# Kernel tuning notes

Measured on AMD Instinct MI355X. Metric: run time of the kernel, lower is better.

## Reference

```python
import jax, jax.numpy as jnp
import numpy as np

B, S, H, HD = 8, 1024, 16, 64
D = H * HD
NINF = -10000.0
EPS = 1e-6


def setup_inputs() -> dict:
    key = jax.random.key(0)
    ks = jax.random.split(key, 6)
    std = 0.02
    return {
        "x": jax.random.normal(ks[0], (B, S, D), jnp.float32),
        "mask": jax.random.randint(ks[1], (B, S), 0, 2, jnp.int32),
        "wq": jax.random.normal(ks[2], (D, D), jnp.float32) * std,
        "bq": jnp.zeros((D,), jnp.float32),
        "wk": jax.random.normal(ks[3], (D, D), jnp.float32) * std,
        "bk": jnp.zeros((D,), jnp.float32),
        "wv": jax.random.normal(ks[4], (D, D), jnp.float32) * std,
        "bv": jnp.zeros((D,), jnp.float32),
        "wo": jax.random.normal(ks[5], (D, D), jnp.float32) * std,
        "bo": jnp.zeros((D,), jnp.float32),
        "gamma": jnp.ones((D,), jnp.float32),
        "beta": jnp.zeros((D,), jnp.float32),
    }


def _heads(t):
    # [B,S,D] -> [B,H,S,HD]
    return t.reshape(t.shape[0], t.shape[1], H, HD).transpose(0, 2, 1, 3)


def _layernorm(x, gamma, beta):
    mu = jnp.mean(x, -1, keepdims=True)
    var = jnp.mean(jnp.square(x - mu), -1, keepdims=True)
    return (x - mu) * jax.lax.rsqrt(var + EPS) * gamma + beta


def reference(x, mask, wq, bq, wk, bk, wv, bv, wo, bo, gamma, beta):
    q = _heads(x @ wq + bq)
    k = _heads(x @ wk + bk)
    v = _heads(x @ wv + bv)
    scores = jnp.einsum("bhqd,bhkd->bhqk", q, k) / np.sqrt(HD).astype(np.float32)
    # padding mask broadcast over key axis: 1 = masked
    scores = scores + mask.astype(jnp.float32)[:, None, None, :] * NINF
    attn = jax.nn.softmax(scores, axis=-1)
    ctx = jnp.einsum("bhqk,bhkd->bhqd", attn, v)  # [B,H,S,HD]
    ctx = ctx.transpose(0, 2, 1, 3).reshape(B, S, D)
    out = _layernorm(x + ctx @ wo + bo, gamma, beta)
    return out
```

## Files before the change

### kernel.cpp

```cpp
#include <hip/hip_runtime.h>
#include <stdint.h>

typedef unsigned short u16;
typedef unsigned int u32;
typedef __bf16 b16x8 __attribute__((ext_vector_type(8)));
typedef float f32x4 __attribute__((ext_vector_type(4)));

#define B_ 8
#define S_ 1024
#define H_ 16
#define HD_ 64
#define D_ 1024
#define M_ 8192

__device__ __forceinline__ u16 f2bf(float f) {
  u32 u = __float_as_uint(f);
  return (u16)((u + 0x7fffu + ((u >> 16) & 1u)) >> 16);
}
__device__ __forceinline__ u16 bfbits(float f) {
  union {
    __bf16 b;
    u16 u;
  } c;
  c.b = (__bf16)f;
  return c.u;
}

__device__ __forceinline__ f32x4 mfma16(b16x8 a, b16x8 b, f32x4 c) {
  return __builtin_amdgcn_mfma_f32_16x16x32_bf16(a, b, c, 0, 0, 0);
}

__device__ __forceinline__ void cp16(const u16* g, u16* l) {
  __builtin_amdgcn_global_load_lds(
      (const __attribute__((address_space(1))) u32*)(g),
      (__attribute__((address_space(3))) u32*)(l), 16, 0, 0);
}

__global__ __launch_bounds__(1024) void wconv_kernel(
    const float* __restrict__ w0, const float* __restrict__ w1,
    const float* __restrict__ w2, const float* __restrict__ w3,
    u16* __restrict__ t0, u16* __restrict__ t1, u16* __restrict__ t2,
    u16* __restrict__ t3) {
  __shared__ float tile[32][33];
  const int z = blockIdx.z;
  const float* src = (z == 0) ? w0 : (z == 1) ? w1 : (z == 2) ? w2 : w3;
  u16* dst = (z == 0) ? t0 : (z == 1) ? t1 : (z == 2) ? t2 : t3;
  const int tx = threadIdx.x, ty = threadIdx.y;
  const int x0 = blockIdx.x * 32, y0 = blockIdx.y * 32;
  tile[ty][tx] = src[(size_t)(y0 + ty) * D_ + x0 + tx];
  __syncthreads();
  dst[(size_t)(x0 + ty) * D_ + y0 + tx] = f2bf(tile[tx][ty]);
}

__global__ __launch_bounds__(256) void xconv_kernel(const float* __restrict__ x,
                                                    u16* __restrict__ xb) {
  const size_t i = ((size_t)blockIdx.x * 256 + threadIdx.x) * 4;
  const float4 v = *(const float4*)(x + i);
  u16 o[4] = {f2bf(v.x), f2bf(v.y), f2bf(v.z), f2bf(v.w)};
  uint2 pack;
  pack.x = ((u32)o[1] << 16) | o[0];
  pack.y = ((u32)o[3] << 16) | o[2];
  *(uint2*)(xb + i) = pack;
}

__device__ __forceinline__ void gemm128_mainloop(
    const u16* __restrict__ A, const u16* __restrict__ BT, int K, int m0,
    int n0, u16* lds, f32x4 (&acc)[4][4]) {
  const int t = threadIdx.x;
  const int lane = t & 63;
  const int w = t >> 6;
  const int l15 = lane & 15;
  const int q4 = lane >> 4;
  const int mwave = (w >> 1) * 64;
  const int nwave = (w & 1) * 64;

  u16* Alds = lds;
  u16* Blds = lds + 8192;

  const f32x4 zero = {0.f, 0.f, 0.f, 0.f};
  for (int mt = 0; mt < 4; ++mt)
    for (int nt = 0; nt < 4; ++nt) acc[mt][nt] = zero;

  const int rbase = t >> 3;
  const int scol = ((t & 7) ^ (rbase & 7)) * 8;
  const u16* Ag = A + (size_t)(m0 + rbase) * K + scol;
  const u16* Bg = BT + (size_t)(n0 + rbase) * K + scol;

  const int sx = l15 & 7;
  const int cA0 = ((0 * 4 + q4) ^ sx) * 8;
  const int cA1 = ((1 * 4 + q4) ^ sx) * 8;

  for (int k0 = 0; k0 < K; k0 += 64) {
    __syncthreads();
    for (int c = 0; c < 4; ++c) {
      cp16(Ag + (size_t)(c * 32) * K + k0, Alds + c * 2048 + t * 8);
      cp16(Bg + (size_t)(c * 32) * K + k0, Blds + c * 2048 + t * 8);
    }
    __syncthreads();

    b16x8 af[4][2], bfr[4][2];
    for (int mt = 0; mt < 4; ++mt) {
      const int row = (mwave + mt * 16 + l15) * 64;
      af[mt][0] = *(const b16x8*)(Alds + row + cA0);
      af[mt][1] = *(const b16x8*)(Alds + row + cA1);
    }
    for (int nt = 0; nt < 4; ++nt) {
      const int row = (nwave + nt * 16 + l15) * 64;
      bfr[nt][0] = *(const b16x8*)(Blds + row + cA0);
      bfr[nt][1] = *(const b16x8*)(Blds + row + cA1);
    }
    for (int mt = 0; mt < 4; ++mt)
      for (int nt = 0; nt < 4; ++nt) {
        acc[mt][nt] = mfma16(af[mt][0], bfr[nt][0], acc[mt][nt]);
        acc[mt][nt] = mfma16(af[mt][1], bfr[nt][1], acc[mt][nt]);
      }
  }
}

__global__ __launch_bounds__(256) void qkv_gemm_kernel(
    const u16* __restrict__ xb, const u16* __restrict__ wtq,
    const u16* __restrict__ wtk, const u16* __restrict__ wtv,
    const float* __restrict__ bq, const float* __restrict__ bk,
    const float* __restrict__ bv, u16* __restrict__ Q, u16* __restrict__ Kb,
    u16* __restrict__ VT) {
  __shared__ __align__(16) u16 lds[16384];
  const int z = blockIdx.z;
  const u16* BTp = (z == 0) ? wtq : (z == 1) ? wtk : wtv;
  const float* bias = (z == 0) ? bq : (z == 1) ? bk : bv;
  u16* out = (z == 0) ? Q : (z == 1) ? Kb : VT;
  const int m0 = blockIdx.y * 128, n0 = blockIdx.x * 128;

  f32x4 acc[4][4];
  gemm128_mainloop(xb, BTp, D_, m0, n0, lds, acc);

  const int lane = threadIdx.x & 63, w = threadIdx.x >> 6;
  const int l15 = lane & 15, q4 = lane >> 4;
  const int mwave = (w >> 1) * 64, nwave = (w & 1) * 64;

  for (int nt = 0; nt < 4; ++nt) {
    const int n = n0 + nwave + nt * 16 + l15;
    const float bias_v = bias[n];
    const int h = n >> 6, hd = n & 63;
    for (int mt = 0; mt < 4; ++mt) {
      for (int r = 0; r < 4; ++r) {
        const int m = m0 + mwave + mt * 16 + q4 * 4 + r;
        const int b = m >> 10, s = m & 1023;
        const float v = acc[mt][nt][r] + bias_v;
        size_t idx;
        if (z < 2)
          idx = (((size_t)(b * H_ + h)) * S_ + s) * HD_ + hd;
        else
          idx = (((size_t)(b * H_ + h)) * HD_ + hd) * S_ + s;
        out[idx] = f2bf(v);
      }
    }
  }
}

#define PAD_ 68
#define QPAD_ 72
__global__ __launch_bounds__(256) void attn_kernel(
    const u16* __restrict__ Q, const u16* __restrict__ Kb,
    const u16* __restrict__ VT, const int* __restrict__ mask,
    u16* __restrict__ ctx) {
  __shared__ __align__(16) u16 QPlds[64 * QPAD_];
  __shared__ __align__(16) u16 Klds[64 * PAD_];
  __shared__ __align__(16) u16 Vlds[64 * PAD_];
  __shared__ __align__(16) float Mlds[1024];

  const int t = threadIdx.x;
  const int lane = t & 63, w = t >> 6;
  const int l15 = lane & 15, q4 = lane >> 4;
  const int id = blockIdx.x;
  const int bh = id & 127;
  const int b = bh >> 4, h = bh & 15;
  const int q0 = (id >> 7) * 64;

  const u16* Qbh = Q + (size_t)bh * S_ * HD_;
  const u16* Kbh = Kb + (size_t)bh * S_ * HD_;
  const u16* Vbh = VT + (size_t)bh * S_ * HD_;
  const int* maskb = mask + b * S_;

  const int srow = t >> 3, scol = (t & 7) * 8;
  {
    b16x8 q0v = *(const b16x8*)(Qbh + (size_t)(q0 + srow) * HD_ + scol);
    b16x8 q1v = *(const b16x8*)(Qbh + (size_t)(q0 + srow + 32) * HD_ + scol);
    const int4 mv = *(const int4*)(maskb + t * 4);
    *(b16x8*)(QPlds + srow * QPAD_ + scol) = q0v;
    *(b16x8*)(QPlds + (srow + 32) * QPAD_ + scol) = q1v;
    float4 mf;
    mf.x = -14427.0f * (float)mv.x;
    mf.y = -14427.0f * (float)mv.y;
    mf.z = -14427.0f * (float)mv.z;
    mf.w = -14427.0f * (float)mv.w;
    *(float4*)(Mlds + t * 4) = mf;
  }
  __syncthreads();
  b16x8 aq[2];
  aq[0] = *(const b16x8*)(QPlds + (w * 16 + l15) * QPAD_ + q4 * 8);
  aq[1] = *(const b16x8*)(QPlds + (w * 16 + l15) * QPAD_ + 32 + q4 * 8);

  const f32x4 zero = {0.f, 0.f, 0.f, 0.f};
  f32x4 acc[4];
  for (int nt = 0; nt < 4; ++nt) acc[nt] = zero;
  float lsum = 0.f;
  u16* Pw = QPlds + w * 16 * QPAD_;
  const float c1 = 0.18033688f;

  b16x8 kv0 = *(const b16x8*)(Kbh + (size_t)srow * HD_ + scol);
  b16x8 kv1 = *(const b16x8*)(Kbh + (size_t)(srow + 32) * HD_ + scol);
  b16x8 vv0 = *(const b16x8*)(Vbh + (size_t)srow * S_ + scol);
  b16x8 vv1 = *(const b16x8*)(Vbh + (size_t)(srow + 32) * S_ + scol);

  for (int j = 0; j < 16; ++j) {
    const int key0 = j * 64;
    __syncthreads();
    *(b16x8*)(Klds + srow * PAD_ + scol) = kv0;
    *(b16x8*)(Klds + (srow + 32) * PAD_ + scol) = kv1;
    *(b16x8*)(Vlds + srow * PAD_ + scol) = vv0;
    *(b16x8*)(Vlds + (srow + 32) * PAD_ + scol) = vv1;
    __syncthreads();

    if (j < 15) {
      const int kn = key0 + 64;
      kv0 = *(const b16x8*)(Kbh + (size_t)(kn + srow) * HD_ + scol);
      kv1 = *(const b16x8*)(Kbh + (size_t)(kn + srow + 32) * HD_ + scol);
      vv0 = *(const b16x8*)(Vbh + (size_t)srow * S_ + kn + scol);
      vv1 = *(const b16x8*)(Vbh + (size_t)(srow + 32) * S_ + kn + scol);
    }

    f32x4 sf[4];
    for (int nt = 0; nt < 4; ++nt) sf[nt] = zero;
    for (int kk = 0; kk < 2; ++kk)
      for (int nt = 0; nt < 4; ++nt) {
        b16x8 bk =
            *(const b16x8*)(Klds + (nt * 16 + l15) * PAD_ + kk * 32 + q4 * 8);
        sf[nt] = mfma16(bk, aq[kk], sf[nt]);
      }

    for (int nt = 0; nt < 4; ++nt) {
      const float4 mk = *(const float4*)(Mlds + key0 + nt * 16 + q4 * 4);
      float p0 = __builtin_amdgcn_exp2f(sf[nt][0] * c1 + mk.x);
      float p1 = __builtin_amdgcn_exp2f(sf[nt][1] * c1 + mk.y);
      float p2 = __builtin_amdgcn_exp2f(sf[nt][2] * c1 + mk.z);
      float p3 = __builtin_amdgcn_exp2f(sf[nt][3] * c1 + mk.w);
      lsum += (p0 + p1) + (p2 + p3);
      uint2 pk;
      pk.x = ((u32)bfbits(p1) << 16) | bfbits(p0);
      pk.y = ((u32)bfbits(p3) << 16) | bfbits(p2);
      *(uint2*)(Pw + l15 * QPAD_ + nt * 16 + q4 * 4) = pk;
    }
    asm volatile("s_waitcnt lgkmcnt(0)" ::: "memory");

    for (int kk = 0; kk < 2; ++kk) {
      b16x8 bp = *(const b16x8*)(Pw + l15 * QPAD_ + kk * 32 + q4 * 8);
      for (int nt = 0; nt < 4; ++nt) {
        b16x8 vb =
            *(const b16x8*)(Vlds + (nt * 16 + l15) * PAD_ + kk * 32 + q4 * 8);
        acc[nt] = mfma16(vb, bp, acc[nt]);
      }
    }
  }

  lsum += __shfl_xor(lsum, 16);
  lsum += __shfl_xor(lsum, 32);
  const float inv = 1.0f / lsum;

  const int srw = q0 + w * 16 + l15;
  u16* crow = ctx + ((size_t)(b * S_ + srw)) * D_ + h * 64;
  for (int nt = 0; nt < 4; ++nt) {
    uint2 pk;
    pk.x = ((u32)bfbits(acc[nt][1] * inv) << 16) | bfbits(acc[nt][0] * inv);
    pk.y = ((u32)bfbits(acc[nt][3] * inv) << 16) | bfbits(acc[nt][2] * inv);
    *(uint2*)(crow + nt * 16 + q4 * 4) = pk;
  }
}

__global__ __launch_bounds__(256) void out_gemm_kernel(
    const u16* __restrict__ ctx, const u16* __restrict__ wto,
    const float* __restrict__ bo, const float* __restrict__ x,
    float* __restrict__ y) {
  __shared__ __align__(16) u16 lds[16384];
  const int m0 = blockIdx.y * 128, n0 = blockIdx.x * 128;
  f32x4 acc[4][4];
  gemm128_mainloop(ctx, wto, D_, m0, n0, lds, acc);

  const int lane = threadIdx.x & 63, w = threadIdx.x >> 6;
  const int l15 = lane & 15, q4 = lane >> 4;
  const int mwave = (w >> 1) * 64, nwave = (w & 1) * 64;

  for (int nt = 0; nt < 4; ++nt) {
    const int n = n0 + nwave + nt * 16 + l15;
    const float bias = bo[n];
    for (int mt = 0; mt < 4; ++mt) {
      for (int r = 0; r < 4; ++r) {
        const int m = m0 + mwave + mt * 16 + q4 * 4 + r;
        y[(size_t)m * D_ + n] = acc[mt][nt][r] + bias + x[(size_t)m * D_ + n];
      }
    }
  }
}

__global__ __launch_bounds__(256) void ln_kernel(const float* __restrict__ y,
                                                 const float* __restrict__ g,
                                                 const float* __restrict__ be,
                                                 float* __restrict__ out) {
  const int row = blockIdx.x, t = threadIdx.x;
  const float* yr = y + (size_t)row * D_;
  const float4 v = *(const float4*)(yr + t * 4);
  float s = v.x + v.y + v.z + v.w;
  float ss = v.x * v.x + v.y * v.y + v.z * v.z + v.w * v.w;
  for (int off = 1; off < 64; off <<= 1) {
    s += __shfl_xor(s, off);
    ss += __shfl_xor(ss, off);
  }
  __shared__ float red[8];
  const int w = t >> 6, lane = t & 63;
  if (lane == 0) {
    red[w] = s;
    red[4 + w] = ss;
  }
  __syncthreads();
  s = red[0] + red[1] + red[2] + red[3];
  ss = red[4] + red[5] + red[6] + red[7];
  const float mu = s * (1.f / 1024.f);
  const float var = ss * (1.f / 1024.f) - mu * mu;
  const float rs = rsqrtf(var + 1e-6f);
  const int c = t * 4;
  const float4 gv = *(const float4*)(g + c);
  const float4 bv = *(const float4*)(be + c);
  float4 o;
  o.x = (v.x - mu) * rs * gv.x + bv.x;
  o.y = (v.y - mu) * rs * gv.y + bv.y;
  o.z = (v.z - mu) * rs * gv.z + bv.z;
  o.w = (v.w - mu) * rs * gv.w + bv.w;
  *(float4*)(out + (size_t)row * D_ + c) = o;
}

extern "C" void kernel_launch(void* const* d_in, const int* in_sizes, int n_in,
                              void* d_out, int out_size, void* d_ws,
                              size_t ws_size, hipStream_t stream) {
  const float* x = (const float*)d_in[0];
  const int* mask = (const int*)d_in[1];
  const float* wq = (const float*)d_in[2];
  const float* bq = (const float*)d_in[3];
  const float* wk = (const float*)d_in[4];
  const float* bk = (const float*)d_in[5];
  const float* wv = (const float*)d_in[6];
  const float* bv = (const float*)d_in[7];
  const float* wo = (const float*)d_in[8];
  const float* bo = (const float*)d_in[9];
  const float* gamma = (const float*)d_in[10];
  const float* beta = (const float*)d_in[11];
  float* out = (float*)d_out;

  char* ws = (char*)d_ws;
  const size_t MB = 1024ull * 1024ull;
  u16* wtq = (u16*)(ws + 0 * MB);
  u16* wtk = (u16*)(ws + 2 * MB);
  u16* wtv = (u16*)(ws + 4 * MB);
  u16* wto = (u16*)(ws + 6 * MB);
  u16* xb = (u16*)(ws + 8 * MB);
  u16* ctx = (u16*)(ws + 8 * MB);
  u16* Qb = (u16*)(ws + 24 * MB);
  u16* Kb = (u16*)(ws + 40 * MB);
  u16* VTb = (u16*)(ws + 56 * MB);
  float* y = (float*)(ws + 24 * MB);

  wconv_kernel<<<dim3(32, 32, 4), dim3(32, 32), 0, stream>>>(
      wq, wk, wv, wo, wtq, wtk, wtv, wto);
  xconv_kernel<<<8192, 256, 0, stream>>>(x, xb);
  qkv_gemm_kernel<<<dim3(8, 64, 3), 256, 0, stream>>>(
      xb, wtq, wtk, wtv, bq, bk, bv, Qb, Kb, VTb);
  attn_kernel<<<2048, 256, 0, stream>>>(Qb, Kb, VTb, mask, ctx);
  out_gemm_kernel<<<dim3(8, 64), 256, 0, stream>>>(ctx, wto, bo, x, y);
  ln_kernel<<<8192, 256, 0, stream>>>(y, gamma, beta, out);
}
```

Baseline: 306.8 us.

## Use triple-buffered 256x128 GEMM tiles with 512 threads and swizzled block order

Replaces the 128x128 single-buffered GEMM mainloop with a 256x128 tile, 8 waves and a 3-stage LDS ring that prefetches two k-tiles ahead, using explicit vmcnt waits and setprio around MFMA bursts. The QKV GEMM now treats the three weight matrices as one concatenated N=3072 operand (wtq is assumed contiguous with wtk and wtv in the workspace), and both GEMMs use a swizzled 1D grid for L2 locality. The aim is to hide global-load latency and cut per-tile synchronization. In exchange it raises LDS use to about 144 KB per block and adds register pressure, which may limit occupancy.

After: 309.9 us. No clear change (+1.0%).

```diff
diff --git a/kernel.cpp b/kernel.cpp
--- a/kernel.cpp
+++ b/kernel.cpp
@@ -63,87 +63,129 @@
   *(uint2*)(xb + i) = pack;
 }
 
-__device__ __forceinline__ void gemm128_mainloop(
+#define BM_ 256
+#define BN_ 128
+#define BK_ 64
+#define ABUF_ 16384
+#define BBUF_ 8192
+#define BUFSZ_ (ABUF_ + BBUF_)
+
+__device__ __forceinline__ void gemm256x128_mainloop(
     const u16* __restrict__ A, const u16* __restrict__ BT, int K, int m0,
-    int n0, u16* lds, f32x4 (&acc)[4][4]) {
+    int n0, u16* lds, f32x4 (&acc)[8][2]) {
   const int t = threadIdx.x;
   const int lane = t & 63;
-  const int w = t >> 6;
   const int l15 = lane & 15;
   const int q4 = lane >> 4;
-  const int mwave = (w >> 1) * 64;
-  const int nwave = (w & 1) * 64;
-
-  u16* Alds = lds;
-  u16* Blds = lds + 8192;
+  const int w = t >> 6;
+  const int wm = w >> 2;
+  const int wn = w & 3;
 
   const f32x4 zero = {0.f, 0.f, 0.f, 0.f};
-  for (int mt = 0; mt < 4; ++mt)
-    for (int nt = 0; nt < 4; ++nt) acc[mt][nt] = zero;
+#pragma unroll
+  for (int mt = 0; mt < 8; ++mt)
+#pragma unroll
+    for (int nt = 0; nt < 2; ++nt) acc[mt][nt] = zero;
 
   const int rbase = t >> 3;
   const int scol = ((t & 7) ^ (rbase & 7)) * 8;
   const u16* Ag = A + (size_t)(m0 + rbase) * K + scol;
   const u16* Bg = BT + (size_t)(n0 + rbase) * K + scol;
-
   const int sx = l15 & 7;
-  const int cA0 = ((0 * 4 + q4) ^ sx) * 8;
-  const int cA1 = ((1 * 4 + q4) ^ sx) * 8;
-
-  for (int k0 = 0; k0 < K; k0 += 64) {
-    __syncthreads();
-    for (int c = 0; c < 4; ++c) {
-      cp16(Ag + (size_t)(c * 32) * K + k0, Alds + c * 2048 + t * 8);
-      cp16(Bg + (size_t)(c * 32) * K + k0, Blds + c * 2048 + t * 8);
-    }
-    __syncthreads();
-
-    b16x8 af[4][2], bfr[4][2];
-    for (int mt = 0; mt < 4; ++mt) {
-      const int row = (mwave + mt * 16 + l15) * 64;
-      af[mt][0] = *(const b16x8*)(Alds + row + cA0);
-      af[mt][1] = *(const b16x8*)(Alds + row + cA1);
-    }
-    for (int nt = 0; nt < 4; ++nt) {
-      const int row = (nwave + nt * 16 + l15) * 64;
-      bfr[nt][0] = *(const b16x8*)(Blds + row + cA0);
-      bfr[nt][1] = *(const b16x8*)(Blds + row + cA1);
-    }
-    for (int mt = 0; mt < 4; ++mt)
-      for (int nt = 0; nt < 4; ++nt) {
-        acc[mt][nt] = mfma16(af[mt][0], bfr[nt][0], acc[mt][nt]);
-        acc[mt][nt] = mfma16(af[mt][1], bfr[nt][1], acc[mt][nt]);
+
+  auto STAGE = [&](int kt, int bufi) {
+    u16* Ab = lds + bufi * BUFSZ_;
+    u16* Bb = Ab + ABUF_;
+    const int k0 = kt * BK_;
+#pragma unroll
+    for (int c = 0; c < 4; ++c)
+      cp16(Ag + (size_t)(c * 64) * K + k0, Ab + c * 4096 + t * 8);
+#pragma unroll
+    for (int c = 0; c < 2; ++c)
+      cp16(Bg + (size_t)(c * 64) * K + k0, Bb + c * 4096 + t * 8);
+  };
+
+  const int NT = K / BK_;
+  STAGE(0, 0);
+  STAGE(1, 1);
+
+  int cur = 0;
+  for (int kt = 0; kt < NT; ++kt) {
+    if (kt + 2 < NT) {
+      int nb = cur + 2;
+      if (nb >= 3) nb -= 3;
+      STAGE(kt + 2, nb);
+    }
+    if (kt + 2 < NT)
+      asm volatile("s_waitcnt vmcnt(12)" ::: "memory");
+    else if (kt + 1 < NT)
+      asm volatile("s_waitcnt vmcnt(6)" ::: "memory");
+    else
+      asm volatile("s_waitcnt vmcnt(0)" ::: "memory");
+    asm volatile("s_barrier" ::: "memory");
+
+    const u16* Ab = lds + cur * BUFSZ_;
+    const u16* Bb = Ab + ABUF_;
+
+#pragma unroll
+    for (int kk = 0; kk < 2; ++kk) {
+      b16x8 af[8], bf2[2];
+      const int cc = ((kk * 4 + q4) ^ sx) * 8;
+#pragma unroll
+      for (int mt = 0; mt < 8; ++mt)
+        af[mt] = *(const b16x8*)(Ab + (wm * 128 + mt * 16 + l15) * 64 + cc);
+#pragma unroll
+      for (int nt = 0; nt < 2; ++nt)
+        bf2[nt] = *(const b16x8*)(Bb + (wn * 32 + nt * 16 + l15) * 64 + cc);
+      asm volatile("s_barrier" ::: "memory");
+      __builtin_amdgcn_s_setprio(1);
+#pragma unroll
+      for (int mt = 0; mt < 8; ++mt) {
+        acc[mt][0] = mfma16(af[mt], bf2[0], acc[mt][0]);
+        acc[mt][1] = mfma16(af[mt], bf2[1], acc[mt][1]);
       }
-  }
-}
-
-__global__ __launch_bounds__(256) void qkv_gemm_kernel(
-    const u16* __restrict__ xb, const u16* __restrict__ wtq,
-    const u16* __restrict__ wtk, const u16* __restrict__ wtv,
+      __builtin_amdgcn_s_setprio(0);
+      asm volatile("s_barrier" ::: "memory");
+    }
+    ++cur;
+    if (cur == 3) cur = 0;
+  }
+}
+
+__global__ __launch_bounds__(512, 2) void qkv_gemm_kernel(
+    const u16* __restrict__ xb, const u16* __restrict__ wt3,
     const float* __restrict__ bq, const float* __restrict__ bk,
     const float* __restrict__ bv, u16* __restrict__ Q, u16* __restrict__ Kb,
     u16* __restrict__ VT) {
-  __shared__ __align__(16) u16 lds[16384];
-  const int z = blockIdx.z;
-  const u16* BTp = (z == 0) ? wtq : (z == 1) ? wtk : wtv;
+  __shared__ __align__(16) u16 lds[3 * BUFSZ_];
+  const int wg = blockIdx.x;
+  const int swz = (wg & 7) * 96 + (wg >> 3);
+  const int by = swz / 24, bx = swz % 24;
+  const int m0 = by * 256;
+  const int n0 = bx * 128;
+
+  f32x4 acc[8][2];
+  gemm256x128_mainloop(xb, wt3, D_, m0, n0, lds, acc);
+
+  const int t = threadIdx.x;
+  const int lane = t & 63, w = t >> 6;
+  const int l15 = lane & 15, q4 = lane >> 4;
+  const int wm = w >> 2, wn = w & 3;
+
+  const int z = n0 >> 10;
+  const u16* dummy;
+  u16* out = (z == 0) ? Q : (z == 1) ? Kb : VT;
   const float* bias = (z == 0) ? bq : (z == 1) ? bk : bv;
-  u16* out = (z == 0) ? Q : (z == 1) ? Kb : VT;
-  const int m0 = blockIdx.y * 128, n0 = blockIdx.x * 128;
-
-  f32x4 acc[4][4];
-  gemm128_mainloop(xb, BTp, D_, m0, n0, lds, acc);
-
-  const int lane = threadIdx.x & 63, w = threadIdx.x >> 6;
-  const int l15 = lane & 15, q4 = lane >> 4;
-  const int mwave = (w >> 1) * 64, nwave = (w & 1) * 64;
-
-  for (int nt = 0; nt < 4; ++nt) {
-    const int n = n0 + nwave + nt * 16 + l15;
-    const float bias_v = bias[n];
-    const int h = n >> 6, hd = n & 63;
-    for (int mt = 0; mt < 4; ++mt) {
+  (void)dummy;
+
+  for (int nt = 0; nt < 2; ++nt) {
+    const int nf = n0 + wn * 32 + nt * 16 + l15;
+    const int n1 = nf & 1023;
+    const float bias_v = bias[n1];
+    const int h = n1 >> 6, hd = n1 & 63;
+    for (int mt = 0; mt < 8; ++mt) {
       for (int r = 0; r < 4; ++r) {
-        const int m = m0 + mwave + mt * 16 + q4 * 4 + r;
+        const int m = m0 + wm * 128 + mt * 16 + q4 * 4 + r;
         const int b = m >> 10, s = m & 1023;
         const float v = acc[mt][nt][r] + bias_v;
         size_t idx;
@@ -276,25 +318,30 @@
   }
 }
 
-__global__ __launch_bounds__(256) void out_gemm_kernel(
+__global__ __launch_bounds__(512, 2) void out_gemm_kernel(
     const u16* __restrict__ ctx, const u16* __restrict__ wto,
     const float* __restrict__ bo, const float* __restrict__ x,
     float* __restrict__ y) {
-  __shared__ __align__(16) u16 lds[16384];
-  const int m0 = blockIdx.y * 128, n0 = blockIdx.x * 128;
-  f32x4 acc[4][4];
-  gemm128_mainloop(ctx, wto, D_, m0, n0, lds, acc);
-
-  const int lane = threadIdx.x & 63, w = threadIdx.x >> 6;
+  __shared__ __align__(16) u16 lds[3 * BUFSZ_];
+  const int wg = blockIdx.x;
+  const int swz = (wg & 7) * 32 + (wg >> 3);
+  const int by = swz / 8, bx = swz % 8;
+  const int m0 = by * 256, n0 = bx * 128;
+
+  f32x4 acc[8][2];
+  gemm256x128_mainloop(ctx, wto, D_, m0, n0, lds, acc);
+
+  const int t = threadIdx.x;
+  const int lane = t & 63, w = t >> 6;
   const int l15 = lane & 15, q4 = lane >> 4;
-  const int mwave = (w >> 1) * 64, nwave = (w & 1) * 64;
-
-  for (int nt = 0; nt < 4; ++nt) {
-    const int n = n0 + nwave + nt * 16 + l15;
+  const int wm = w >> 2, wn = w & 3;
+
+  for (int nt = 0; nt < 2; ++nt) {
+    const int n = n0 + wn * 32 + nt * 16 + l15;
     const float bias = bo[n];
-    for (int mt = 0; mt < 4; ++mt) {
+    for (int mt = 0; mt < 8; ++mt) {
       for (int r = 0; r < 4; ++r) {
-        const int m = m0 + mwave + mt * 16 + q4 * 4 + r;
+        const int m = m0 + wm * 128 + mt * 16 + q4 * 4 + r;
         y[(size_t)m * D_ + n] = acc[mt][nt][r] + bias + x[(size_t)m * D_ + n];
       }
     }
@@ -370,9 +417,8 @@
   wconv_kernel<<<dim3(32, 32, 4), dim3(32, 32), 0, stream>>>(
       wq, wk, wv, wo, wtq, wtk, wtv, wto);
   xconv_kernel<<<8192, 256, 0, stream>>>(x, xb);
-  qkv_gemm_kernel<<<dim3(8, 64, 3), 256, 0, stream>>>(
-      xb, wtq, wtk, wtv, bq, bk, bv, Qb, Kb, VTb);
+  qkv_gemm_kernel<<<768, 512, 0, stream>>>(xb, wtq, bq, bk, bv, Qb, Kb, VTb);
   attn_kernel<<<2048, 256, 0, stream>>>(Qb, Kb, VTb, mask, ctx);
-  out_gemm_kernel<<<dim3(8, 64), 256, 0, stream>>>(ctx, wto, bo, x, y);
+  out_gemm_kernel<<<256, 512, 0, stream>>>(ctx, wto, bo, x, y);
   ln_kernel<<<8192, 256, 0, stream>>>(y, gamma, beta, out);
 }
```
